# Optimization experiments

Measured on AMD Instinct MI355X. Metric: run time of the kernel, lower is better.

## Reference

```python
import jax, jax.numpy as jnp
import numpy as np

B, N, HID = 2, 2048, 1024
NH = 16
HD = HID // NH

def setup_inputs() -> dict:
    key = jax.random.key(0)
    ks = jax.random.split(key, 5)
    s = 0.02
    return {
        "hidden_states": jax.random.normal(ks[0], (B, N, HID), jnp.float32),
        "attention_mask": jnp.zeros((B, 1, 1, N), jnp.float32),
        "Wq": jax.random.normal(ks[1], (HID, HID), jnp.float32) * s,
        "bq": jnp.zeros((HID,), jnp.float32),
        "Wk": jax.random.normal(ks[2], (HID, HID), jnp.float32) * s,
        "bk": jnp.zeros((HID,), jnp.float32),
        "Wv": jax.random.normal(ks[3], (HID, HID), jnp.float32) * s,
        "bv": jnp.zeros((HID,), jnp.float32),
    }

def reference(hidden_states, attention_mask, Wq, bq, Wk, bk, Wv, bv):
    b, n, _ = hidden_states.shape
    def split_heads(t):  # [b,n,hid] -> [b,h,n,d]
        return t.reshape(b, n, NH, HD).transpose(0, 2, 1, 3)
    q = split_heads(hidden_states @ Wq.T + bq)
    k = split_heads(hidden_states @ Wk.T + bk)
    v = split_heads(hidden_states @ Wv.T + bv)
    scores = jnp.einsum('bhnd,bhmd->bhnm', q, k) / jnp.sqrt(jnp.float32(HD)).astype(q.dtype)
    scores = scores + attention_mask
    scores = jnp.maximum(scores, jnp.finfo(scores.dtype).min)
    probs = jax.nn.softmax(scores, axis=-1)
    out = jnp.einsum('bhnm,bhmd->bhnd', probs, v)
    return out.transpose(0, 2, 1, 3).reshape(b, n, NH * HD)
```

## Files before the change

### kernel.cpp

```cpp
#include <hip/hip_runtime.h>

typedef unsigned short u16;
typedef unsigned int   u32;
typedef __attribute__((ext_vector_type(8))) short bf16x8;
typedef __attribute__((ext_vector_type(4))) float f32x4;

__device__ __forceinline__ float bf2f(u16 u) { return __uint_as_float(((u32)u) << 16); }
__device__ __forceinline__ u16 f2bf(float f) {
    return (u16)((__float_as_uint(f) + 0x8000u) >> 16);
}
__device__ __forceinline__ void gload16(const void* g, void* l) {
    __builtin_amdgcn_global_load_lds((const __attribute__((address_space(1))) void*)g,
                                     (__attribute__((address_space(3))) void*)l, 16, 0, 0);
}

struct us4 { u16 x, y, z, w; };
__global__ void cvt_all(const float* __restrict__ hs, const float* __restrict__ wq,
                        const float* __restrict__ wk, const float* __restrict__ wv,
                        u16* __restrict__ dst)
{
    int i = blockIdx.x * blockDim.x + threadIdx.x;
    const int stride = gridDim.x * blockDim.x;
    us4* d4 = (us4*)dst;
    for (; i < 1835008; i += stride) {
        const float4* s4;
        int j = i;
        if (j < 1048576)      { s4 = (const float4*)hs; }
        else if (j < 1310720) { s4 = (const float4*)wq; j -= 1048576; }
        else if (j < 1572864) { s4 = (const float4*)wk; j -= 1310720; }
        else                  { s4 = (const float4*)wv; j -= 1572864; }
        float4 v = s4[j];
        us4 o;
        o.x = f2bf(v.x); o.y = f2bf(v.y); o.z = f2bf(v.z); o.w = f2bf(v.w);
        d4[i] = o;
    }
}

__global__ __launch_bounds__(256) void qkv_gemm(
    const u16* __restrict__ hs,
    const u16* __restrict__ Wq, const u16* __restrict__ Wk, const u16* __restrict__ Wv,
    const float* __restrict__ bq, const float* __restrict__ bk, const float* __restrict__ bv,
    u16* __restrict__ oq, u16* __restrict__ ok, u16* __restrict__ ovt)
{
    __shared__ u16 smem[20480];
    u16* sA = smem;
    u16* sB = smem + 8192;

    const int tid  = threadIdx.x;
    const int lane = tid & 63;
    const int wv_  = tid >> 6;
    const int c15  = lane & 15;
    const int q4   = lane >> 4;
    const int rb   = blockIdx.x;
    const int mat  = blockIdx.y >> 3;
    const int cb   = blockIdx.y & 7;

    const u16*   W    = (mat == 0) ? Wq : (mat == 1 ? Wk : Wv);
    const float* bias = (mat == 0) ? bq : (mat == 1 ? bk : bv);

    const int wr = wv_ >> 1, wc = wv_ & 1;

    f32x4 acc[4][4] = {};

    int rowS[4], colS[4];
#pragma unroll
    for (int p = 0; p < 4; ++p) {
        const int ch = p * 256 + tid;
        rowS[p] = ch >> 3;
        colS[p] = ((ch & 7) ^ (rowS[p] & 7)) * 8;
    }
    const u16* gA = hs + (rb * 128) * 1024;
    const u16* gB = W + (cb * 128) * 1024;
    const int swz = c15 & 7;

    for (int kb = 0; kb < 1024; kb += 64) {
        __syncthreads();
#pragma unroll
        for (int p = 0; p < 4; ++p) {
            u16* lA = sA + (p * 256 + wv_ * 64) * 8;
            u16* lB = sB + (p * 256 + wv_ * 64) * 8;
            gload16(gA + rowS[p] * 1024 + kb + colS[p], lA);
            gload16(gB + rowS[p] * 1024 + kb + colS[p], lB);
        }
        __syncthreads();

#pragma unroll
        for (int kk = 0; kk < 2; ++kk) {
            bf16x8 af[4], bf[4];
#pragma unroll
            for (int mt = 0; mt < 4; ++mt) {
                const int row = wr * 64 + mt * 16 + c15;
                af[mt] = *(const bf16x8*)(sA + row * 64 + (((kk * 4 + q4) ^ swz) * 8));
            }
#pragma unroll
            for (int nt = 0; nt < 4; ++nt) {
                const int row = wc * 64 + nt * 16 + c15;
                bf[nt] = *(const bf16x8*)(sB + row * 64 + (((kk * 4 + q4) ^ swz) * 8));
            }
#pragma unroll
            for (int mt = 0; mt < 4; ++mt)
#pragma unroll
                for (int nt = 0; nt < 4; ++nt)
                    acc[mt][nt] = __builtin_amdgcn_mfma_f32_16x16x32_bf16(
                        af[mt], bf[nt], acc[mt][nt], 0, 0, 0);
        }
    }

    __syncthreads();
    const int hcol = (cb * 128 + wc * 64) >> 6;
    float bvv[4];
#pragma unroll
    for (int nt = 0; nt < 4; ++nt)
        bvv[nt] = bias[cb * 128 + wc * 64 + nt * 16 + c15];

    if (mat != 2) {
        u16* dst = (mat == 0) ? oq : ok;
#pragma unroll
        for (int mh = 0; mh < 2; ++mh) {
            u16* sc = smem + wv_ * 5120 + mh * 2304;
#pragma unroll
            for (int mt2 = 0; mt2 < 2; ++mt2) {
                const int mt = mh * 2 + mt2;
#pragma unroll
                for (int nt = 0; nt < 4; ++nt)
#pragma unroll
                    for (int r = 0; r < 4; ++r)
                        sc[(mt2 * 16 + q4 * 4 + r) * 72 + nt * 16 + c15] =
                            f2bf(acc[mt][nt][r] + bvv[nt]);
            }
#pragma unroll
            for (int i = 0; i < 4; ++i) {
                const int rl = i * 8 + (lane >> 3);
                const int d0 = (lane & 7) * 8;
                bf16x8 vv = *(const bf16x8*)(sc + rl * 72 + d0);
                const int n = rb * 128 + wr * 64 + mh * 32 + rl;
                const int bb = n >> 11, nn = n & 2047;
                *(bf16x8*)(dst + (((bb * 16 + hcol) * 2048) + nn) * 64 + d0) = vv;
            }
        }
    } else {
#pragma unroll
        for (int mh = 0; mh < 2; ++mh) {
            u16* sc = smem + wv_ * 5120 + mh * 2560;
#pragma unroll
            for (int mt2 = 0; mt2 < 2; ++mt2) {
                const int mt = mh * 2 + mt2;
#pragma unroll
                for (int nt = 0; nt < 4; ++nt)
#pragma unroll
                    for (int r = 0; r < 4; ++r)
                        sc[(nt * 16 + c15) * 40 + mt2 * 16 + q4 * 4 + r] =
                            f2bf(acc[mt][nt][r] + bvv[nt]);
            }
#pragma unroll
            for (int i = 0; i < 4; ++i) {
                const int dp = i * 16 + (lane >> 2);
                const int nl = (lane & 3) * 8;
                bf16x8 vv = *(const bf16x8*)(sc + dp * 40 + nl);
                const int n = rb * 128 + wr * 64 + mh * 32 + nl;
                const int bb = n >> 11, nn = n & 2047;
                *(bf16x8*)(ovt + (((bb * 16 + hcol) * 64) + dp) * 2048 + nn) = vv;
            }
        }
    }
}

__global__ __launch_bounds__(256) void attn(
    const u16* __restrict__ qm, const u16* __restrict__ km, const u16* __restrict__ vtm,
    const float* __restrict__ mask, float* __restrict__ out)
{
    __shared__ u16 sK[2][64 * 64];
    __shared__ u16 sVT[2][64 * 64];
    __shared__ u16 sP[4][16 * 72];

    const int tid = threadIdx.x, lane = tid & 63, w = tid >> 6;
    const int c15 = lane & 15, q4 = lane >> 4;
    const int qt = blockIdx.x;
    const int bh = blockIdx.y;
    const int b = bh >> 4;

    bf16x8 qf[2];
    const u16* qbase = qm + (bh * 2048 + qt * 64 + w * 16) * 64;
#pragma unroll
    for (int kt = 0; kt < 2; ++kt)
        qf[kt] = *(const bf16x8*)(qbase + c15 * 64 + kt * 32 + q4 * 8);

    float l_acc[4] = {0.f, 0.f, 0.f, 0.f};
    f32x4 accO[4] = {};

    const u16* kbase  = km  + bh * 2048 * 64;
    const u16* vtbase = vtm + bh * 64 * 2048;

    const int ch0 = tid, ch1 = 256 + tid;
    const int r0 = ch0 >> 3, cc0 = ((ch0 & 7) ^ (r0 & 7)) * 8;
    const int r1 = ch1 >> 3, cc1 = ((ch1 & 7) ^ (r1 & 7)) * 8;

    for (int it = 0; it < 16; ++it) {
        const int kb = it * 128;
        __syncthreads();

#pragma unroll
        for (int half = 0; half < 2; ++half) {
            u16* lk0 = sK[half]  + (w * 64) * 8;
            u16* lk1 = sK[half]  + (256 + w * 64) * 8;
            u16* lv0 = sVT[half] + (w * 64) * 8;
            u16* lv1 = sVT[half] + (256 + w * 64) * 8;
            const int ko = kb + half * 64;
            gload16(kbase + (ko + r0) * 64 + cc0, lk0);
            gload16(kbase + (ko + r1) * 64 + cc1, lk1);
            gload16(vtbase + r0 * 2048 + ko + cc0, lv0);
            gload16(vtbase + r1 * 2048 + ko + cc1, lv1);
        }
        __syncthreads();

#pragma unroll
        for (int half = 0; half < 2; ++half) {
            const u16* cK = sK[half];
            const u16* cV = sVT[half];
            const int kpos = kb + half * 64;

            float mk[4];
#pragma unroll
            for (int nt = 0; nt < 4; ++nt)
                mk[nt] = mask[b * 2048 + kpos + nt * 16 + c15];

            f32x4 accS[4] = {};
#pragma unroll
            for (int kt = 0; kt < 2; ++kt) {
                bf16x8 kf[4];
#pragma unroll
                for (int nt = 0; nt < 4; ++nt) {
                    const int key = nt * 16 + c15;
                    const int cpos = (q4 + 4 * kt) ^ (key & 7);
                    kf[nt] = *(const bf16x8*)(cK + key * 64 + cpos * 8);
                }
#pragma unroll
                for (int nt = 0; nt < 4; ++nt)
                    accS[nt] = __builtin_amdgcn_mfma_f32_16x16x32_bf16(
                        qf[kt], kf[nt], accS[nt], 0, 0, 0);
            }

#pragma unroll
            for (int nt = 0; nt < 4; ++nt)
#pragma unroll
                for (int r = 0; r < 4; ++r) {
                    const float p = __expf(fmaf(accS[nt][r], 0.125f, mk[nt]));
                    l_acc[r] += p;
                    sP[w][(q4 * 4 + r) * 72 + nt * 16 + c15] = f2bf(p);
                }


#pragma unroll
            for (int kt = 0; kt < 2; ++kt) {
                bf16x8 pf = *(const bf16x8*)(&sP[w][c15 * 72 + kt * 32 + q4 * 8]);
                bf16x8 vf[4];
#pragma unroll
                for (int nt = 0; nt < 4; ++nt) {
                    const int d = nt * 16 + c15;
                    const int cpos = (kt * 4 + q4) ^ (d & 7);
                    vf[nt] = *(const bf16x8*)(cV + d * 64 + cpos * 8);
                }
#pragma unroll
                for (int nt = 0; nt < 4; ++nt)
                    accO[nt] = __builtin_amdgcn_mfma_f32_16x16x32_bf16(
                        pf, vf[nt], accO[nt], 0, 0, 0);
            }
        }
    }

#pragma unroll
    for (int off = 1; off < 16; off <<= 1)
#pragma unroll
        for (int r = 0; r < 4; ++r)
            l_acc[r] += __shfl_xor(l_acc[r], off);

    const int h = bh & 15;
    float inv[4];
#pragma unroll
    for (int r = 0; r < 4; ++r) inv[r] = 1.0f / l_acc[r];
#pragma unroll
    for (int nt = 0; nt < 4; ++nt)
#pragma unroll
        for (int r = 0; r < 4; ++r) {
            const int qrow = qt * 64 + w * 16 + q4 * 4 + r;
            const int d = nt * 16 + c15;
            out[(b * 2048 + qrow) * 1024 + h * 64 + d] = accO[nt][r] * inv[r];
        }
}

extern "C" void kernel_launch(void* const* d_in, const int* in_sizes, int n_in,
                              void* d_out, int out_size, void* d_ws, size_t ws_size,
                              hipStream_t stream)
{
    const float* hs   = (const float*)d_in[0];
    const float* mask = (const float*)d_in[1];
    const float* Wq   = (const float*)d_in[2];
    const float* bq   = (const float*)d_in[3];
    const float* Wk   = (const float*)d_in[4];
    const float* bk   = (const float*)d_in[5];
    const float* Wv   = (const float*)d_in[6];
    const float* bv   = (const float*)d_in[7];

    u16* ws   = (u16*)d_ws;
    u16* qw   = ws;
    u16* kw   = ws + 4194304;
    u16* vtw  = ws + 8388608;
    u16* hsb  = ws + 12582912;
    u16* wqb  = ws + 16777216;
    u16* wkb  = ws + 17825792;
    u16* wvb  = ws + 18874368;

    cvt_all<<<1024, 256, 0, stream>>>(hs, Wq, Wk, Wv, hsb);

    qkv_gemm<<<dim3(32, 24), 256, 0, stream>>>(hsb, wqb, wkb, wvb, bq, bk, bv, qw, kw, vtw);
    attn<<<dim3(32, 32), 256, 0, stream>>>(qw, kw, vtw, mask, (float*)d_out);
}
```

Baseline: 197.5 us.

## Retile QKV GEMM to 64x128 blocks and attention to 128-query tiles

The QKV projection GEMM now uses 64-row by 128-column tiles, with each wave owning 32 output columns, which doubles the grid to 1536 blocks for better CU occupancy. The attention kernel now processes 128 queries per block (32 per wave, two row tiles), so each K/V tile loaded into LDS is reused across twice as many queries and K/V global traffic is halved. Its K/V staging drops from two 64-key halves per iteration to one 64-key tile. The trade-offs are more accumulator registers per wave in attention and only 512 attention blocks, so fewer waves are available to hide latency.

After: 180.5 us. 1.09x faster.

```diff
diff --git a/kernel.cpp b/kernel.cpp
--- a/kernel.cpp
+++ b/kernel.cpp
@@ -42,9 +42,9 @@
     const float* __restrict__ bq, const float* __restrict__ bk, const float* __restrict__ bv,
     u16* __restrict__ oq, u16* __restrict__ ok, u16* __restrict__ ovt)
 {
-    __shared__ u16 smem[20480];
+    __shared__ u16 smem[12288];
     u16* sA = smem;
-    u16* sB = smem + 8192;
+    u16* sB = smem + 4096;
 
     const int tid  = threadIdx.x;
     const int lane = tid & 63;
@@ -58,109 +58,97 @@
     const u16*   W    = (mat == 0) ? Wq : (mat == 1 ? Wk : Wv);
     const float* bias = (mat == 0) ? bq : (mat == 1 ? bk : bv);
 
-    const int wr = wv_ >> 1, wc = wv_ & 1;
-
-    f32x4 acc[4][4] = {};
-
-    int rowS[4], colS[4];
+    f32x4 acc[4][2] = {};
+
+    int rA[2], cA[2], rB[4], cB[4];
+#pragma unroll
+    for (int p = 0; p < 2; ++p) {
+        const int ch = p * 256 + tid;
+        rA[p] = ch >> 3; cA[p] = ((ch & 7) ^ (rA[p] & 7)) * 8;
+    }
 #pragma unroll
     for (int p = 0; p < 4; ++p) {
         const int ch = p * 256 + tid;
-        rowS[p] = ch >> 3;
-        colS[p] = ((ch & 7) ^ (rowS[p] & 7)) * 8;
-    }
-    const u16* gA = hs + (rb * 128) * 1024;
+        rB[p] = ch >> 3; cB[p] = ((ch & 7) ^ (rB[p] & 7)) * 8;
+    }
+    const u16* gA = hs + (rb * 64) * 1024;
     const u16* gB = W + (cb * 128) * 1024;
     const int swz = c15 & 7;
 
     for (int kb = 0; kb < 1024; kb += 64) {
         __syncthreads();
 #pragma unroll
-        for (int p = 0; p < 4; ++p) {
-            u16* lA = sA + (p * 256 + wv_ * 64) * 8;
-            u16* lB = sB + (p * 256 + wv_ * 64) * 8;
-            gload16(gA + rowS[p] * 1024 + kb + colS[p], lA);
-            gload16(gB + rowS[p] * 1024 + kb + colS[p], lB);
-        }
+        for (int p = 0; p < 2; ++p)
+            gload16(gA + rA[p] * 1024 + kb + cA[p], sA + (p * 256 + wv_ * 64) * 8);
+#pragma unroll
+        for (int p = 0; p < 4; ++p)
+            gload16(gB + rB[p] * 1024 + kb + cB[p], sB + (p * 256 + wv_ * 64) * 8);
         __syncthreads();
 
 #pragma unroll
         for (int kk = 0; kk < 2; ++kk) {
-            bf16x8 af[4], bf[4];
-#pragma unroll
-            for (int mt = 0; mt < 4; ++mt) {
-                const int row = wr * 64 + mt * 16 + c15;
-                af[mt] = *(const bf16x8*)(sA + row * 64 + (((kk * 4 + q4) ^ swz) * 8));
-            }
-#pragma unroll
-            for (int nt = 0; nt < 4; ++nt) {
-                const int row = wc * 64 + nt * 16 + c15;
-                bf[nt] = *(const bf16x8*)(sB + row * 64 + (((kk * 4 + q4) ^ swz) * 8));
-            }
+            const int cpos = ((kk * 4 + q4) ^ swz) * 8;
+            bf16x8 af[4], bf[2];
 #pragma unroll
             for (int mt = 0; mt < 4; ++mt)
-#pragma unroll
-                for (int nt = 0; nt < 4; ++nt)
+                af[mt] = *(const bf16x8*)(sA + (mt * 16 + c15) * 64 + cpos);
+#pragma unroll
+            for (int nt = 0; nt < 2; ++nt)
+                bf[nt] = *(const bf16x8*)(sB + (wv_ * 32 + nt * 16 + c15) * 64 + cpos);
+#pragma unroll
+            for (int mt = 0; mt < 4; ++mt)
+#pragma unroll
+                for (int nt = 0; nt < 2; ++nt)
                     acc[mt][nt] = __builtin_amdgcn_mfma_f32_16x16x32_bf16(
                         af[mt], bf[nt], acc[mt][nt], 0, 0, 0);
         }
     }
 
     __syncthreads();
-    const int hcol = (cb * 128 + wc * 64) >> 6;
-    float bvv[4];
-#pragma unroll
-    for (int nt = 0; nt < 4; ++nt)
-        bvv[nt] = bias[cb * 128 + wc * 64 + nt * 16 + c15];
-
+    const int hcol = cb * 2 + (wv_ >> 1);
+    const int dbase = (wv_ & 1) * 32;
+    float bvv[2];
+#pragma unroll
+    for (int nt = 0; nt < 2; ++nt)
+        bvv[nt] = bias[cb * 128 + wv_ * 32 + nt * 16 + c15];
+
+    u16* sc = smem + wv_ * 2560;
     if (mat != 2) {
         u16* dst = (mat == 0) ? oq : ok;
 #pragma unroll
-        for (int mh = 0; mh < 2; ++mh) {
-            u16* sc = smem + wv_ * 5120 + mh * 2304;
-#pragma unroll
-            for (int mt2 = 0; mt2 < 2; ++mt2) {
-                const int mt = mh * 2 + mt2;
-#pragma unroll
-                for (int nt = 0; nt < 4; ++nt)
-#pragma unroll
-                    for (int r = 0; r < 4; ++r)
-                        sc[(mt2 * 16 + q4 * 4 + r) * 72 + nt * 16 + c15] =
-                            f2bf(acc[mt][nt][r] + bvv[nt]);
-            }
-#pragma unroll
-            for (int i = 0; i < 4; ++i) {
-                const int rl = i * 8 + (lane >> 3);
-                const int d0 = (lane & 7) * 8;
-                bf16x8 vv = *(const bf16x8*)(sc + rl * 72 + d0);
-                const int n = rb * 128 + wr * 64 + mh * 32 + rl;
-                const int bb = n >> 11, nn = n & 2047;
-                *(bf16x8*)(dst + (((bb * 16 + hcol) * 2048) + nn) * 64 + d0) = vv;
-            }
+        for (int mt = 0; mt < 4; ++mt)
+#pragma unroll
+            for (int nt = 0; nt < 2; ++nt)
+#pragma unroll
+                for (int r = 0; r < 4; ++r)
+                    sc[(mt * 16 + q4 * 4 + r) * 40 + nt * 16 + c15] =
+                        f2bf(acc[mt][nt][r] + bvv[nt]);
+#pragma unroll
+        for (int i = 0; i < 4; ++i) {
+            const int rl = i * 16 + (lane >> 2);
+            const int c0 = (lane & 3) * 8;
+            bf16x8 vv = *(const bf16x8*)(sc + rl * 40 + c0);
+            const int n = rb * 64 + rl;
+            const int bb = n >> 11, nn = n & 2047;
+            *(bf16x8*)(dst + (((bb * 16 + hcol) * 2048) + nn) * 64 + dbase + c0) = vv;
         }
     } else {
 #pragma unroll
-        for (int mh = 0; mh < 2; ++mh) {
-            u16* sc = smem + wv_ * 5120 + mh * 2560;
-#pragma unroll
-            for (int mt2 = 0; mt2 < 2; ++mt2) {
-                const int mt = mh * 2 + mt2;
-#pragma unroll
-                for (int nt = 0; nt < 4; ++nt)
-#pragma unroll
-                    for (int r = 0; r < 4; ++r)
-                        sc[(nt * 16 + c15) * 40 + mt2 * 16 + q4 * 4 + r] =
-                            f2bf(acc[mt][nt][r] + bvv[nt]);
-            }
-#pragma unroll
-            for (int i = 0; i < 4; ++i) {
-                const int dp = i * 16 + (lane >> 2);
-                const int nl = (lane & 3) * 8;
-                bf16x8 vv = *(const bf16x8*)(sc + dp * 40 + nl);
-                const int n = rb * 128 + wr * 64 + mh * 32 + nl;
-                const int bb = n >> 11, nn = n & 2047;
-                *(bf16x8*)(ovt + (((bb * 16 + hcol) * 64) + dp) * 2048 + nn) = vv;
-            }
+        for (int mt = 0; mt < 4; ++mt)
+#pragma unroll
+            for (int nt = 0; nt < 2; ++nt)
+#pragma unroll
+                for (int r = 0; r < 4; ++r)
+                    sc[(nt * 16 + c15) * 72 + mt * 16 + q4 * 4 + r] =
+                        f2bf(acc[mt][nt][r] + bvv[nt]);
+#pragma unroll
+        for (int i = 0; i < 4; ++i) {
+            const int dp = i * 8 + (lane >> 3);
+            const int nl = (lane & 7) * 8;
+            bf16x8 vv = *(const bf16x8*)(sc + dp * 72 + nl);
+            const int n = rb * 64 + nl;
+            const int bb = n >> 11, nn = n & 2047;
+            *(bf16x8*)(ovt + (((bb * 16 + hcol) * 64) + dbase + dp) * 2048 + nn) = vv;
         }
     }
 }
@@ -169,9 +157,9 @@
     const u16* __restrict__ qm, const u16* __restrict__ km, const u16* __restrict__ vtm,
     const float* __restrict__ mask, float* __restrict__ out)
 {
-    __shared__ u16 sK[2][64 * 64];
-    __shared__ u16 sVT[2][64 * 64];
-    __shared__ u16 sP[4][16 * 72];
+    __shared__ u16 sK[64 * 64];
+    __shared__ u16 sVT[64 * 64];
+    __shared__ u16 sP[4][32 * 72];
 
     const int tid = threadIdx.x, lane = tid & 63, w = tid >> 6;
     const int c15 = lane & 15, q4 = lane >> 4;
@@ -179,113 +167,112 @@
     const int bh = blockIdx.y;
     const int b = bh >> 4;
 
-    bf16x8 qf[2];
-    const u16* qbase = qm + (bh * 2048 + qt * 64 + w * 16) * 64;
-#pragma unroll
-    for (int kt = 0; kt < 2; ++kt)
-        qf[kt] = *(const bf16x8*)(qbase + c15 * 64 + kt * 32 + q4 * 8);
-
-    float l_acc[4] = {0.f, 0.f, 0.f, 0.f};
-    f32x4 accO[4] = {};
+    bf16x8 qf[2][2];
+    const u16* qbase = qm + (bh * 2048 + qt * 128 + w * 32) * 64;
+#pragma unroll
+    for (int rt = 0; rt < 2; ++rt)
+#pragma unroll
+        for (int kt = 0; kt < 2; ++kt)
+            qf[rt][kt] = *(const bf16x8*)(qbase + (rt * 16 + c15) * 64 + kt * 32 + q4 * 8);
+
+    float l_acc[2][4] = {};
+    f32x4 accO[2][4] = {};
 
     const u16* kbase  = km  + bh * 2048 * 64;
     const u16* vtbase = vtm + bh * 64 * 2048;
 
-    const int ch0 = tid, ch1 = 256 + tid;
-    const int r0 = ch0 >> 3, cc0 = ((ch0 & 7) ^ (r0 & 7)) * 8;
-    const int r1 = ch1 >> 3, cc1 = ((ch1 & 7) ^ (r1 & 7)) * 8;
-
-    for (int it = 0; it < 16; ++it) {
-        const int kb = it * 128;
+    const int r0 = tid >> 3,         cc0 = ((tid & 7) ^ (r0 & 7)) * 8;
+    const int r1 = (256 + tid) >> 3, cc1 = ((tid & 7) ^ (r1 & 7)) * 8;
+
+    for (int it = 0; it < 32; ++it) {
+        const int kb = it * 64;
         __syncthreads();
 
-#pragma unroll
-        for (int half = 0; half < 2; ++half) {
-            u16* lk0 = sK[half]  + (w * 64) * 8;
-            u16* lk1 = sK[half]  + (256 + w * 64) * 8;
-            u16* lv0 = sVT[half] + (w * 64) * 8;
-            u16* lv1 = sVT[half] + (256 + w * 64) * 8;
-            const int ko = kb + half * 64;
-            gload16(kbase + (ko + r0) * 64 + cc0, lk0);
-            gload16(kbase + (ko + r1) * 64 + cc1, lk1);
-            gload16(vtbase + r0 * 2048 + ko + cc0, lv0);
-            gload16(vtbase + r1 * 2048 + ko + cc1, lv1);
-        }
+        gload16(kbase + (kb + r0) * 64 + cc0, sK + (w * 64) * 8);
+        gload16(kbase + (kb + r1) * 64 + cc1, sK + (256 + w * 64) * 8);
+        gload16(vtbase + r0 * 2048 + kb + cc0, sVT + (w * 64) * 8);
+        gload16(vtbase + r1 * 2048 + kb + cc1, sVT + (256 + w * 64) * 8);
         __syncthreads();
 
-#pragma unroll
-        for (int half = 0; half < 2; ++half) {
-            const u16* cK = sK[half];
-            const u16* cV = sVT[half];
-            const int kpos = kb + half * 64;
-
-            float mk[4];
+        float mk[4];
+#pragma unroll
+        for (int nt = 0; nt < 4; ++nt)
+            mk[nt] = mask[b * 2048 + kb + nt * 16 + c15];
+
+        f32x4 accS[2][4] = {};
+#pragma unroll
+        for (int kt = 0; kt < 2; ++kt) {
+            bf16x8 kf[4];
+#pragma unroll
+            for (int nt = 0; nt < 4; ++nt) {
+                const int key = nt * 16 + c15;
+                const int cpos = (q4 + 4 * kt) ^ (key & 7);
+                kf[nt] = *(const bf16x8*)(sK + key * 64 + cpos * 8);
+            }
+#pragma unroll
+            for (int rt = 0; rt < 2; ++rt)
+#pragma unroll
+                for (int nt = 0; nt < 4; ++nt)
+                    accS[rt][nt] = __builtin_amdgcn_mfma_f32_16x16x32_bf16(
+                        qf[rt][kt], kf[nt], accS[rt][nt], 0, 0, 0);
+        }
+
+#pragma unroll
+        for (int rt = 0; rt < 2; ++rt)
 #pragma unroll
             for (int nt = 0; nt < 4; ++nt)
-                mk[nt] = mask[b * 2048 + kpos + nt * 16 + c15];
-
-            f32x4 accS[4] = {};
-#pragma unroll
-            for (int kt = 0; kt < 2; ++kt) {
-                bf16x8 kf[4];
-#pragma unroll
-                for (int nt = 0; nt < 4; ++nt) {
-                    const int key = nt * 16 + c15;
-                    const int cpos = (q4 + 4 * kt) ^ (key & 7);
-                    kf[nt] = *(const bf16x8*)(cK + key * 64 + cpos * 8);
+#pragma unroll
+                for (int r = 0; r < 4; ++r) {
+                    const float p = __expf(fmaf(accS[rt][nt][r], 0.125f, mk[nt]));
+                    l_acc[rt][r] += p;
+                    sP[w][(rt * 16 + q4 * 4 + r) * 72 + nt * 16 + c15] = f2bf(p);
                 }
+
+
+#pragma unroll
+        for (int kt = 0; kt < 2; ++kt) {
+            bf16x8 pf[2], vf[4];
+#pragma unroll
+            for (int rt = 0; rt < 2; ++rt)
+                pf[rt] = *(const bf16x8*)(&sP[w][(rt * 16 + c15) * 72 + kt * 32 + q4 * 8]);
+#pragma unroll
+            for (int nt = 0; nt < 4; ++nt) {
+                const int d = nt * 16 + c15;
+                const int cpos = (kt * 4 + q4) ^ (d & 7);
+                vf[nt] = *(const bf16x8*)(sVT + d * 64 + cpos * 8);
+            }
+#pragma unroll
+            for (int rt = 0; rt < 2; ++rt)
 #pragma unroll
                 for (int nt = 0; nt < 4; ++nt)
-                    accS[nt] = __builtin_amdgcn_mfma_f32_16x16x32_bf16(
-                        qf[kt], kf[nt], accS[nt], 0, 0, 0);
+                    accO[rt][nt] = __builtin_amdgcn_mfma_f32_16x16x32_bf16(
+                        pf[rt], vf[nt], accO[rt][nt], 0, 0, 0);
+        }
+    }
+
+#pragma unroll
+    for (int off = 1; off < 16; off <<= 1)
+#pragma unroll
+        for (int rt = 0; rt < 2; ++rt)
+#pragma unroll
+            for (int r = 0; r < 4; ++r)
+                l_acc[rt][r] += __shfl_xor(l_acc[rt][r], off);
+
+    const int h = bh & 15;
+#pragma unroll
+    for (int rt = 0; rt < 2; ++rt) {
+        float inv[4];
+#pragma unroll
+        for (int r = 0; r < 4; ++r) inv[r] = 1.0f / l_acc[rt][r];
+#pragma unroll
+        for (int nt = 0; nt < 4; ++nt)
+#pragma unroll
+            for (int r = 0; r < 4; ++r) {
+                const int qrow = qt * 128 + w * 32 + rt * 16 + q4 * 4 + r;
+                const int d = nt * 16 + c15;
+                out[(b * 2048 + qrow) * 1024 + h * 64 + d] = accO[rt][nt][r] * inv[r];
             }
-
-#pragma unroll
-            for (int nt = 0; nt < 4; ++nt)
-#pragma unroll
-                for (int r = 0; r < 4; ++r) {
-                    const float p = __expf(fmaf(accS[nt][r], 0.125f, mk[nt]));
-                    l_acc[r] += p;
-                    sP[w][(q4 * 4 + r) * 72 + nt * 16 + c15] = f2bf(p);
-                }
-
-
-#pragma unroll
-            for (int kt = 0; kt < 2; ++kt) {
-                bf16x8 pf = *(const bf16x8*)(&sP[w][c15 * 72 + kt * 32 + q4 * 8]);
-                bf16x8 vf[4];
-#pragma unroll
-                for (int nt = 0; nt < 4; ++nt) {
-                    const int d = nt * 16 + c15;
-                    const int cpos = (kt * 4 + q4) ^ (d & 7);
-                    vf[nt] = *(const bf16x8*)(cV + d * 64 + cpos * 8);
-                }
-#pragma unroll
-                for (int nt = 0; nt < 4; ++nt)
-                    accO[nt] = __builtin_amdgcn_mfma_f32_16x16x32_bf16(
-                        pf, vf[nt], accO[nt], 0, 0, 0);
-            }
-        }
-    }
-
-#pragma unroll
-    for (int off = 1; off < 16; off <<= 1)
-#pragma unroll
-        for (int r = 0; r < 4; ++r)
-            l_acc[r] += __shfl_xor(l_acc[r], off);
-
-    const int h = bh & 15;
-    float inv[4];
-#pragma unroll
-    for (int r = 0; r < 4; ++r) inv[r] = 1.0f / l_acc[r];
-#pragma unroll
-    for (int nt = 0; nt < 4; ++nt)
-#pragma unroll
-        for (int r = 0; r < 4; ++r) {
-            const int qrow = qt * 64 + w * 16 + q4 * 4 + r;
-            const int d = nt * 16 + c15;
-            out[(b * 2048 + qrow) * 1024 + h * 64 + d] = accO[nt][r] * inv[r];
-        }
+    }
 }
 
 extern "C" void kernel_launch(void* const* d_in, const int* in_sizes, int n_in,
@@ -312,6 +299,6 @@
 
     cvt_all<<<1024, 256, 0, stream>>>(hs, Wq, Wk, Wv, hsb);
 
-    qkv_gemm<<<dim3(32, 24), 256, 0, stream>>>(hsb, wqb, wkb, wvb, bq, bk, bv, qw, kw, vtw);
-    attn<<<dim3(32, 32), 256, 0, stream>>>(qw, kw, vtw, mask, (float*)d_out);
-}
+    qkv_gemm<<<dim3(64, 24), 256, 0, stream>>>(hsb, wqb, wkb, wvb, bq, bk, bv, qw, kw, vtw);
+    attn<<<dim3(16, 32), 256, 0, stream>>>(qw, kw, vtw, mask, (float*)d_out);
+}
```
